# Performance work log

Hardware: AMD Instinct MI355X
Metric: run time of the kernel (lower is better)

Reference implementation:

```python
import jax, jax.numpy as jnp
import numpy as np

N_NODES = 100000
N_EDGES = 1600000
IN_CH = 128
OUT_CH = 32
HEADS = 2
NEG_SLOPE = 0.2  # GATv2Conv default negative_slope


def setup_inputs() -> dict:
    key = jax.random.key(0)
    ks = jax.random.split(key, 6)
    x = jax.random.normal(ks[0], (N_NODES, IN_CH), dtype=jnp.float32)
    edge_index = jax.random.randint(ks[1], (2, N_EDGES), 0, N_NODES, dtype=jnp.int64)
    s_in = 1.0 / np.sqrt(IN_CH)
    Wl = jax.random.normal(ks[2], (IN_CH, HEADS * OUT_CH), dtype=jnp.float32) * s_in  # lin_l weight
    Wr = jax.random.normal(ks[3], (IN_CH, HEADS * OUT_CH), dtype=jnp.float32) * s_in  # lin_r weight
    bl = jnp.zeros((HEADS * OUT_CH,), dtype=jnp.float32)
    br = jnp.zeros((HEADS * OUT_CH,), dtype=jnp.float32)
    att = jax.random.normal(ks[4], (HEADS, OUT_CH), dtype=jnp.float32) * (1.0 / np.sqrt(OUT_CH))
    bias = jnp.zeros((OUT_CH,), dtype=jnp.float32)  # output bias (concat=False -> size out_channels)
    return {"x": x, "Wl": Wl, "bl": bl, "Wr": Wr, "br": br, "att": att, "bias": bias,
            "edge_index": edge_index}


def _gatv2_layer(x, Wl, bl, Wr, br, att, bias, edge_index):
    N = x.shape[0]
    H, C = att.shape
    # add self loops (GATv2Conv default add_self_loops=True)
    loops = jnp.arange(N, dtype=edge_index.dtype)
    src = jnp.concatenate([edge_index[0], loops])  # [E+N] message sources j
    dst = jnp.concatenate([edge_index[1], loops])  # [E+N] message targets i
    # per-node linear transforms (share_weights=False)
    xl = (x @ Wl + bl).reshape(N, H, C)
    xr = (x @ Wr + br).reshape(N, H, C)
    # GATv2 dynamic attention: a^T LeakyReLU(xl[j] + xr[i])
    h = xl[src] + xr[dst]                                   # [E, H, C]
    e = jnp.einsum('ehc,hc->eh', jax.nn.leaky_relu(h, NEG_SLOPE), att)  # [E, H]
    # segment softmax over incoming edges of each target node
    m = jax.ops.segment_max(e, dst, num_segments=N)         # [N, H]
    a = jnp.exp(e - m[dst])
    denom = jax.ops.segment_sum(a, dst, num_segments=N)     # [N, H]
    alpha = a / (denom[dst] + 1e-16)                        # [E, H]
    # weighted scatter-add of source messages
    out = jax.ops.segment_sum(alpha[:, :, None] * xl[src], dst, num_segments=N)  # [N, H, C]
    out = out.mean(axis=1) + bias                           # concat=False -> head mean
    return jax.nn.silu(out)                                 # activation='silu'


def reference(x, Wl, bl, Wr, br, att, bias, edge_index):
    return _gatv2_layer(x, Wl, bl, Wr, br, att, bias, edge_index)
```

## Files before the change

### kernel.cpp

```cpp
#include <hip/hip_runtime.h>
#include <math.h>

#define BSH 9
#define BMASK ((1 << BSH) - 1)
#define CAP 12288
#define ACH 2048

typedef unsigned int uint;
typedef __attribute__((ext_vector_type(8))) short bf16x8;
typedef __attribute__((ext_vector_type(4))) float f32x4;
typedef __attribute__((ext_vector_type(2))) float f32x2;

static __device__ __forceinline__ unsigned short f2bf(float f) {
    uint u = __float_as_uint(f);
    return (unsigned short)((u + 0x7fffu + ((u >> 16) & 1u)) >> 16);
}

static __device__ __forceinline__ f32x2 dec2(uint u) {
    f32x2 r;
    r.x = __uint_as_float(u << 16);
    r.y = __uint_as_float(u & 0xffff0000u);
    return r;
}

static __device__ __forceinline__ f32x2 abs2(f32x2 h) {
    f32x2 r;
    r.x = __uint_as_float(__float_as_uint(h.x) & 0x7fffffffu);
    r.y = __uint_as_float(__float_as_uint(h.y) & 0x7fffffffu);
    return r;
}

static __device__ __forceinline__ float qsum(float p) {
    p += __uint_as_float(__builtin_amdgcn_mov_dpp(__float_as_uint(p), 0xB1, 0xF, 0xF, true));
    p += __uint_as_float(__builtin_amdgcn_mov_dpp(__float_as_uint(p), 0x4E, 0xF, 0xF, true));
    return p;
}

__global__ __launch_bounds__(256) void k_init(int* __restrict__ bcur, int NB) {
    int i = blockIdx.x * 256 + threadIdx.x;
    if (i < NB) bcur[i] = i * CAP;
}

__global__ __launch_bounds__(256) void k_gemm(const float* __restrict__ x,
        const float* __restrict__ Wl, const float* __restrict__ bl,
        const float* __restrict__ Wr, const float* __restrict__ br,
        unsigned short* __restrict__ xlh, float* __restrict__ xr, int N)
{
    __shared__ __align__(16) char sA[32768];
    __shared__ __align__(16) char sB[32768];
    const int t = threadIdx.x;
    const int base = blockIdx.x * 128;

#pragma unroll 4
    for (int s = 0; s < 16; ++s) {
        int f = s * 256 + t;
        int r = f >> 5;
        int c4 = f & 31;
        int rg = base + r; if (rg >= N) rg = N - 1;
        float4 v = ((const float4*)x)[(size_t)rg * 32 + c4];
        uint2 pk;
        pk.x = (uint)f2bf(v.x) | ((uint)f2bf(v.y) << 16);
        pk.y = (uint)f2bf(v.z) | ((uint)f2bf(v.w) << 16);
        int kb = c4 * 8;
        *(uint2*)(sA + r * 256 + (kb ^ ((r & 7) << 4))) = pk;
    }
#pragma unroll
    for (int s = 0; s < 8; ++s) {
        int tau = s * 256 + t;
        int m  = tau >> 10;
        int k2 = (tau >> 4) & 63;
        int n4 = tau & 15;
        const float4* Wp = (const float4*)(m ? Wr : Wl);
        float4 a = Wp[(2 * k2) * 16 + n4];
        float4 b = Wp[(2 * k2 + 1) * 16 + n4];
        const float* af = (const float*)&a;
        const float* bf = (const float*)&b;
#pragma unroll
        for (int j = 0; j < 4; ++j) {
            int n = m * 64 + n4 * 4 + j;
            uint u = (uint)f2bf(af[j]) | ((uint)f2bf(bf[j]) << 16);
            *(uint*)(sB + n * 256 + ((k2 * 4) ^ ((n & 7) << 4))) = u;
        }
    }
    __syncthreads();

    const int w = t >> 6;
    const int lo = t & 15;
    const int hi = (t & 63) >> 4;
    f32x4 acc[2][8];
#pragma unroll
    for (int f = 0; f < 2; ++f)
#pragma unroll
        for (int j = 0; j < 8; ++j)
            acc[f][j] = (f32x4){0.f, 0.f, 0.f, 0.f};

#pragma unroll
    for (int ks = 0; ks < 4; ++ks) {
        int kb = ks * 64 + hi * 16;
        bf16x8 av[2], bv[8];
#pragma unroll
        for (int f = 0; f < 2; ++f) {
            int r = w * 32 + f * 16 + lo;
            av[f] = *(const bf16x8*)(sA + r * 256 + (kb ^ ((r & 7) << 4)));
        }
#pragma unroll
        for (int j = 0; j < 8; ++j) {
            int nn = j * 16 + lo;
            bv[j] = *(const bf16x8*)(sB + nn * 256 + (kb ^ ((nn & 7) << 4)));
        }
#pragma unroll
        for (int f = 0; f < 2; ++f)
#pragma unroll
            for (int j = 0; j < 8; ++j)
                acc[f][j] = __builtin_amdgcn_mfma_f32_16x16x32_bf16(av[f], bv[j], acc[f][j], 0, 0, 0);
    }

#pragma unroll
    for (int f = 0; f < 2; ++f) {
        int rbase = base + w * 32 + f * 16 + hi * 4;
#pragma unroll
        for (int j = 0; j < 8; ++j) {
            int nn = j * 16 + lo;
            float bvv = (j < 4) ? bl[nn] : br[nn - 64];
            float vv[4] = {acc[f][j][0] + bvv, acc[f][j][1] + bvv,
                           acc[f][j][2] + bvv, acc[f][j][3] + bvv};
            if (j < 4) {
#pragma unroll
                for (int q = 0; q < 4; ++q)
                    if (rbase + q < N) xlh[(size_t)(rbase + q) * 64 + nn] = f2bf(vv[q]);
            } else {
#pragma unroll
                for (int q = 0; q < 4; ++q)
                    if (rbase + q < N) xr[(size_t)(rbase + q) * 64 + (nn - 64)] = vv[q];
            }
        }
    }
}

__global__ __launch_bounds__(256) void k_scatA(const int* __restrict__ ei, int* __restrict__ bcur,
                                               unsigned* __restrict__ pairs, int E, int T, int NB) {
    __shared__ int h[256];
    __shared__ int basem[256];
    int b0 = blockIdx.x * ACH;
    int cnt = min(ACH, T - b0);
    h[threadIdx.x] = 0;
    __syncthreads();
    for (int i = threadIdx.x; i < cnt; i += 256) {
        int t = b0 + i;
        int d = (t < E) ? ei[E + t] : (t - E);
        atomicAdd(&h[d >> BSH], 1);
    }
    __syncthreads();
    if (threadIdx.x < NB) {
        int c = h[threadIdx.x];
        basem[threadIdx.x] = c ? atomicAdd(&bcur[threadIdx.x], c) : 0;
    }
    __syncthreads();
    h[threadIdx.x] = 0;
    __syncthreads();
    for (int i = threadIdx.x; i < cnt; i += 256) {
        int t = b0 + i;
        int s, d;
        if (t < E) { s = ei[t]; d = ei[E + t]; } else { s = t - E; d = s; }
        int b = d >> BSH;
        int idx = atomicAdd(&h[b], 1);
        pairs[basem[b] + idx] = ((unsigned)s << BSH) | (unsigned)(d & BMASK);
    }
}

__global__ __launch_bounds__(512) void k_scatB(const unsigned* __restrict__ pairs,
                                               const int* __restrict__ bcur,
                                               int* __restrict__ src_s, int2* __restrict__ rowrng, int N) {
    __shared__ int cnt[512];
    __shared__ int sm[512];
    __shared__ int lofs[512];
    int b = blockIdx.x;
    int beg = b * CAP, end = bcur[b];
    int nbase = b << BSH;
    cnt[threadIdx.x] = 0;
    __syncthreads();
    for (int i = beg + threadIdx.x; i < end; i += 512)
        atomicAdd(&cnt[pairs[i] & BMASK], 1);
    __syncthreads();
    int v = cnt[threadIdx.x];
    sm[threadIdx.x] = v;
    __syncthreads();
    int acc = v;
    for (int off = 1; off < 512; off <<= 1) {
        int t = (threadIdx.x >= off) ? sm[threadIdx.x - off] : 0;
        __syncthreads();
        acc += t;
        sm[threadIdx.x] = acc;
        __syncthreads();
    }
    int excl = acc - v;
    lofs[threadIdx.x] = excl;
    int n = nbase + threadIdx.x;
    if (n < N) rowrng[n] = make_int2(beg + excl, beg + excl + v);
    cnt[threadIdx.x] = 0;
    __syncthreads();
    for (int i = beg + threadIdx.x; i < end; i += 512) {
        unsigned p = pairs[i];
        int dl = p & BMASK;
        int idx = atomicAdd(&cnt[dl], 1);
        src_s[beg + lofs[dl] + idx] = p >> BSH;
    }
}

__global__ __launch_bounds__(256) void k_fused(const int2* __restrict__ rowrng,
        const int* __restrict__ src_s, const unsigned short* __restrict__ xlh,
        const float* __restrict__ xr, const float* __restrict__ att,
        const float* __restrict__ bias, float* __restrict__ out, int N)
{
    int n = blockIdx.x * 32 + (threadIdx.x >> 3);
    int j = threadIdx.x & 7;
    if (n >= N) return;
    const uint4* xl4 = (const uint4*)xlh;
    f32x2 xr2[4], att2[4];
    {
        float4 a = ((const float4*)xr)[(size_t)n * 16 + j * 2];
        float4 b = ((const float4*)xr)[(size_t)n * 16 + j * 2 + 1];
        xr2[0] = (f32x2){a.x, a.y}; xr2[1] = (f32x2){a.z, a.w};
        xr2[2] = (f32x2){b.x, b.y}; xr2[3] = (f32x2){b.z, b.w};
        float4 c = ((const float4*)att)[j * 2];
        float4 d = ((const float4*)att)[j * 2 + 1];
        att2[0] = (f32x2){c.x, c.y}; att2[1] = (f32x2){c.z, c.w};
        att2[2] = (f32x2){d.x, d.y}; att2[3] = (f32x2){d.z, d.w};
    }
    int2 rr = rowrng[n];
    float ssum = 0.f;
    f32x2 acc2[4] = {(f32x2){0.f,0.f}, (f32x2){0.f,0.f}, (f32x2){0.f,0.f}, (f32x2){0.f,0.f}};

#define EDGE_BODY(u)                                                      \
    {                                                                     \
        f32x2 v0 = dec2((u).x), v1 = dec2((u).y), v2 = dec2((u).z), v3 = dec2((u).w); \
        f32x2 h0 = v0 + xr2[0], h1 = v1 + xr2[1], h2 = v2 + xr2[2], h3 = v3 + xr2[3]; \
        f32x2 pa = h0 * att2[0]; pa += h1 * att2[1]; pa += h2 * att2[2]; pa += h3 * att2[3]; \
        f32x2 pb = abs2(h0) * att2[0]; pb += abs2(h1) * att2[1];          \
        pb += abs2(h2) * att2[2]; pb += abs2(h3) * att2[3];               \
        float p = 0.6f * (pa.x + pa.y) + 0.4f * (pb.x + pb.y);            \
        p = qsum(p);                                                      \
        float wq = __expf(p);                                             \
        ssum += wq;                                                       \
        f32x2 ws = (f32x2){wq, wq};                                       \
        acc2[0] += ws * v0; acc2[1] += ws * v1;                           \
        acc2[2] += ws * v2; acc2[3] += ws * v3;                           \
    }

    int i = rr.x;
    for (; i + 4 <= rr.y; i += 4) {
        int s0 = src_s[i], s1 = src_s[i + 1], s2 = src_s[i + 2], s3 = src_s[i + 3];
        uint4 u0 = xl4[(((uint)s0 << 3) | j)];
        uint4 u1 = xl4[(((uint)s1 << 3) | j)];
        uint4 u2 = xl4[(((uint)s2 << 3) | j)];
        uint4 u3 = xl4[(((uint)s3 << 3) | j)];
        EDGE_BODY(u0); EDGE_BODY(u1); EDGE_BODY(u2); EDGE_BODY(u3);
    }
    for (; i < rr.y; ++i) {
        int s0 = src_s[i];
        uint4 u0 = xl4[(((uint)s0 << 3) | j)];
        EDGE_BODY(u0);
    }
#undef EDGE_BODY

    float inv = 1.f / ssum;
    float o[8];
#pragma unroll
    for (int q = 0; q < 4; ++q) {
        float vx = acc2[q].x * inv, vy = acc2[q].y * inv;
        o[2 * q]     = (vx + __shfl_xor(vx, 4)) * 0.5f;
        o[2 * q + 1] = (vy + __shfl_xor(vy, 4)) * 0.5f;
    }
    if (j < 4) {
        float4 b0 = ((const float4*)bias)[j * 2];
        float4 b1 = ((const float4*)bias)[j * 2 + 1];
        float4 r0, r1;
        r0.x = o[0] + b0.x; r0.y = o[1] + b0.y; r0.z = o[2] + b0.z; r0.w = o[3] + b0.w;
        r1.x = o[4] + b1.x; r1.y = o[5] + b1.y; r1.z = o[6] + b1.z; r1.w = o[7] + b1.w;
        r0.x = r0.x / (1.f + __expf(-r0.x));
        r0.y = r0.y / (1.f + __expf(-r0.y));
        r0.z = r0.z / (1.f + __expf(-r0.z));
        r0.w = r0.w / (1.f + __expf(-r0.w));
        r1.x = r1.x / (1.f + __expf(-r1.x));
        r1.y = r1.y / (1.f + __expf(-r1.y));
        r1.z = r1.z / (1.f + __expf(-r1.z));
        r1.w = r1.w / (1.f + __expf(-r1.w));
        ((float4*)out)[(size_t)n * 8 + j * 2] = r0;
        ((float4*)out)[(size_t)n * 8 + j * 2 + 1] = r1;
    }
}

extern "C" void kernel_launch(void* const* d_in, const int* in_sizes, int n_in,
                              void* d_out, int out_size, void* d_ws, size_t ws_size,
                              hipStream_t stream) {
    const float* x    = (const float*)d_in[0];
    const float* Wl   = (const float*)d_in[1];
    const float* bl   = (const float*)d_in[2];
    const float* Wr   = (const float*)d_in[3];
    const float* br   = (const float*)d_in[4];
    const float* att  = (const float*)d_in[5];
    const float* bias = (const float*)d_in[6];
    const int*   ei   = (const int*)d_in[7];
    float* out = (float*)d_out;

    const int N = in_sizes[0] / 128;
    const int E = in_sizes[7] / 2;
    const int T = E + N;
    const int NB = (N + (1 << BSH) - 1) >> BSH;

    char* p = (char*)d_ws;
    auto take = [&](size_t bytes) {
        char* r = p;
        p += (bytes + 255) & ~(size_t)255;
        return r;
    };
    unsigned short* xlh = (unsigned short*)take((size_t)N * 64 * 2);
    float*    xr     = (float*)take((size_t)N * 64 * 4);
    unsigned* pairs  = (unsigned*)take((size_t)NB * CAP * 4);
    int*      src_s  = (int*)take((size_t)NB * CAP * 4);
    int2*     rowrng = (int2*)take((size_t)N * 8);
    int*      bcur   = (int*)take((size_t)NB * 4);

    k_init <<<1,                   256, 0, stream>>>(bcur, NB);
    k_gemm <<<(N + 127) / 128,     256, 0, stream>>>(x, Wl, bl, Wr, br, xlh, xr, N);
    k_scatA<<<(T + ACH - 1) / ACH, 256, 0, stream>>>(ei, bcur, pairs, E, T, NB);
    k_scatB<<<NB,                  512, 0, stream>>>(pairs, bcur, src_s, rowrng, N);
    k_fused<<<(N + 31) / 32,       256, 0, stream>>>(rowrng, src_s, xlh, xr, att, bias, out, N);
}
```

Baseline: 123.2 us.

## Merge GEMM and edge-bucketing kernels into one launch, deepen edge unroll

The node GEMM and the first edge-bucketing pass now run as one kernel, with the block index choosing the role. This removes a launch and lets the two independent stages overlap on the device. Every block now requests 64KB of dynamic shared memory, including the bucketing blocks that need only about 2KB, which may lower their occupancy. The attention kernel also pre-scales the attention vector by 0.6 and 0.4 to fold the LeakyReLU mixing into one accumulator, and unrolls the gather loop to 8 edges with all loads issued first.

```diff
diff --git a/kernel.cpp b/kernel.cpp
--- a/kernel.cpp
+++ b/kernel.cpp
@@ -41,15 +41,16 @@
     if (i < NB) bcur[i] = i * CAP;
 }
 
-__global__ __launch_bounds__(256) void k_gemm(const float* __restrict__ x,
+static __device__ __forceinline__ void gemm_body(char* smem,
+        const float* __restrict__ x,
         const float* __restrict__ Wl, const float* __restrict__ bl,
         const float* __restrict__ Wr, const float* __restrict__ br,
-        unsigned short* __restrict__ xlh, float* __restrict__ xr, int N)
+        unsigned short* __restrict__ xlh, float* __restrict__ xr, int N, int bid)
 {
-    __shared__ __align__(16) char sA[32768];
-    __shared__ __align__(16) char sB[32768];
+    char* sA = smem;
+    char* sB = smem + 32768;
     const int t = threadIdx.x;
-    const int base = blockIdx.x * 128;
+    const int base = bid * 128;
 
 #pragma unroll 4
     for (int s = 0; s < 16; ++s) {
@@ -137,11 +138,13 @@
     }
 }
 
-__global__ __launch_bounds__(256) void k_scatA(const int* __restrict__ ei, int* __restrict__ bcur,
-                                               unsigned* __restrict__ pairs, int E, int T, int NB) {
-    __shared__ int h[256];
-    __shared__ int basem[256];
-    int b0 = blockIdx.x * ACH;
+static __device__ __forceinline__ void scatA_body(char* smem,
+        const int* __restrict__ ei, int* __restrict__ bcur,
+        unsigned* __restrict__ pairs, int E, int T, int NB, int bid)
+{
+    int* h = (int*)smem;
+    int* basem = h + 256;
+    int b0 = bid * ACH;
     int cnt = min(ACH, T - b0);
     h[threadIdx.x] = 0;
     __syncthreads();
@@ -166,6 +169,20 @@
         int idx = atomicAdd(&h[b], 1);
         pairs[basem[b] + idx] = ((unsigned)s << BSH) | (unsigned)(d & BMASK);
     }
+}
+
+__global__ __launch_bounds__(256) void k_gs(const float* __restrict__ x,
+        const float* __restrict__ Wl, const float* __restrict__ bl,
+        const float* __restrict__ Wr, const float* __restrict__ br,
+        unsigned short* __restrict__ xlh, float* __restrict__ xr, int N,
+        const int* __restrict__ ei, int* __restrict__ bcur,
+        unsigned* __restrict__ pairs, int E, int T, int NB, int GB)
+{
+    extern __shared__ char smem[];
+    if ((int)blockIdx.x < GB)
+        gemm_body(smem, x, Wl, bl, Wr, br, xlh, xr, N, blockIdx.x);
+    else
+        scatA_body(smem, ei, bcur, pairs, E, T, NB, blockIdx.x - GB);
 }
 
 __global__ __launch_bounds__(512) void k_scatB(const unsigned* __restrict__ pairs,
@@ -215,8 +232,8 @@
     int n = blockIdx.x * 32 + (threadIdx.x >> 3);
     int j = threadIdx.x & 7;
     if (n >= N) return;
-    const uint4* xl4 = (const uint4*)xlh;
-    f32x2 xr2[4], att2[4];
+    const uint4* xl4 = (const uint4*)xlh + j;
+    f32x2 xr2[4], a06[4], a04[4];
     {
         float4 a = ((const float4*)xr)[(size_t)n * 16 + j * 2];
         float4 b = ((const float4*)xr)[(size_t)n * 16 + j * 2 + 1];
@@ -224,8 +241,10 @@
         xr2[2] = (f32x2){b.x, b.y}; xr2[3] = (f32x2){b.z, b.w};
         float4 c = ((const float4*)att)[j * 2];
         float4 d = ((const float4*)att)[j * 2 + 1];
-        att2[0] = (f32x2){c.x, c.y}; att2[1] = (f32x2){c.z, c.w};
-        att2[2] = (f32x2){d.x, d.y}; att2[3] = (f32x2){d.z, d.w};
+        a06[0] = (f32x2){0.6f * c.x, 0.6f * c.y}; a06[1] = (f32x2){0.6f * c.z, 0.6f * c.w};
+        a06[2] = (f32x2){0.6f * d.x, 0.6f * d.y}; a06[3] = (f32x2){0.6f * d.z, 0.6f * d.w};
+        a04[0] = (f32x2){0.4f * c.x, 0.4f * c.y}; a04[1] = (f32x2){0.4f * c.z, 0.4f * c.w};
+        a04[2] = (f32x2){0.4f * d.x, 0.4f * d.y}; a04[3] = (f32x2){0.4f * d.z, 0.4f * d.w};
     }
     int2 rr = rowrng[n];
     float ssum = 0.f;
@@ -235,10 +254,10 @@
     {                                                                     \
         f32x2 v0 = dec2((u).x), v1 = dec2((u).y), v2 = dec2((u).z), v3 = dec2((u).w); \
         f32x2 h0 = v0 + xr2[0], h1 = v1 + xr2[1], h2 = v2 + xr2[2], h3 = v3 + xr2[3]; \
-        f32x2 pa = h0 * att2[0]; pa += h1 * att2[1]; pa += h2 * att2[2]; pa += h3 * att2[3]; \
-        f32x2 pb = abs2(h0) * att2[0]; pb += abs2(h1) * att2[1];          \
-        pb += abs2(h2) * att2[2]; pb += abs2(h3) * att2[3];               \
-        float p = 0.6f * (pa.x + pa.y) + 0.4f * (pb.x + pb.y);            \
+        f32x2 pa = h0 * a06[0]; pa += h1 * a06[1]; pa += h2 * a06[2]; pa += h3 * a06[3]; \
+        pa += abs2(h0) * a04[0]; pa += abs2(h1) * a04[1];                 \
+        pa += abs2(h2) * a04[2]; pa += abs2(h3) * a04[3];                 \
+        float p = pa.x + pa.y;                                            \
         p = qsum(p);                                                      \
         float wq = __expf(p);                                             \
         ssum += wq;                                                       \
@@ -248,17 +267,27 @@
     }
 
     int i = rr.x;
-    for (; i + 4 <= rr.y; i += 4) {
-        int s0 = src_s[i], s1 = src_s[i + 1], s2 = src_s[i + 2], s3 = src_s[i + 3];
-        uint4 u0 = xl4[(((uint)s0 << 3) | j)];
-        uint4 u1 = xl4[(((uint)s1 << 3) | j)];
-        uint4 u2 = xl4[(((uint)s2 << 3) | j)];
-        uint4 u3 = xl4[(((uint)s3 << 3) | j)];
-        EDGE_BODY(u0); EDGE_BODY(u1); EDGE_BODY(u2); EDGE_BODY(u3);
+    for (; i + 8 <= rr.y; i += 8) {
+        uint4 u[8];
+#pragma unroll
+        for (int q = 0; q < 8; ++q)
+            u[q] = xl4[((uint)src_s[i + q] << 3)];
+#pragma unroll
+        for (int q = 0; q < 8; ++q)
+            EDGE_BODY(u[q]);
+    }
+    if (i + 4 <= rr.y) {
+        uint4 u[4];
+#pragma unroll
+        for (int q = 0; q < 4; ++q)
+            u[q] = xl4[((uint)src_s[i + q] << 3)];
+#pragma unroll
+        for (int q = 0; q < 4; ++q)
+            EDGE_BODY(u[q]);
+        i += 4;
     }
     for (; i < rr.y; ++i) {
-        int s0 = src_s[i];
-        uint4 u0 = xl4[(((uint)s0 << 3) | j)];
+        uint4 u0 = xl4[((uint)src_s[i] << 3)];
         EDGE_BODY(u0);
     }
 #undef EDGE_BODY
@@ -321,9 +350,11 @@
     int2*     rowrng = (int2*)take((size_t)N * 8);
     int*      bcur   = (int*)take((size_t)NB * 4);
 
-    k_init <<<1,                   256, 0, stream>>>(bcur, NB);
-    k_gemm <<<(N + 127) / 128,     256, 0, stream>>>(x, Wl, bl, Wr, br, xlh, xr, N);
-    k_scatA<<<(T + ACH - 1) / ACH, 256, 0, stream>>>(ei, bcur, pairs, E, T, NB);
-    k_scatB<<<NB,                  512, 0, stream>>>(pairs, bcur, src_s, rowrng, N);
-    k_fused<<<(N + 31) / 32,       256, 0, stream>>>(rowrng, src_s, xlh, xr, att, bias, out, N);
-}
+    const int GB = (N + 127) / 128;
+    const int SB = (T + ACH - 1) / ACH;
+    k_init <<<1,           256, 0, stream>>>(bcur, NB);
+    k_gs   <<<GB + SB,     256, 65536, stream>>>(x, Wl, bl, Wr, br, xlh, xr, N,
+                                                 ei, bcur, pairs, E, T, NB, GB);
+    k_scatB<<<NB,          512, 0, stream>>>(pairs, bcur, src_s, rowrng, N);
+    k_fused<<<(N + 31) / 32, 256, 0, stream>>>(rowrng, src_s, xlh, xr, att, bias, out, N);
+}
```

New measurement: 111.6 us. -9.4%, faster.
